# Optimization experiments

Measured on AMD Instinct MI355X. Metric: run time of the kernel, lower is better.

Reference implementation:

```python
import jax, jax.numpy as jnp
import numpy as np

D = 1024
H = 16
HD = D // H
FF = 4 * D
EPS = 1e-5


def setup_inputs() -> dict:
    key = jax.random.key(0)
    ks = jax.random.split(key, 16)
    s = lambda k, shape, scale: jax.random.normal(k, shape, dtype=jnp.float32) * scale
    inp = {
        "x": s(ks[0], (8, 1024, D), 1.0),
        "Wq": s(ks[1], (D, D), D ** -0.5), "bq": jnp.zeros((D,), jnp.float32),
        "Wk": s(ks[2], (D, D), D ** -0.5), "bk": jnp.zeros((D,), jnp.float32),
        "Wv": s(ks[3], (D, D), D ** -0.5), "bv": jnp.zeros((D,), jnp.float32),
        "Wo": s(ks[4], (D, D), D ** -0.5), "bo": jnp.zeros((D,), jnp.float32),
        "W1": s(ks[5], (D, FF), D ** -0.5), "b1": jnp.zeros((FF,), jnp.float32),
        "W2": s(ks[6], (FF, D), FF ** -0.5), "b2": jnp.zeros((D,), jnp.float32),
        "g1": jnp.ones((D,), jnp.float32), "be1": jnp.zeros((D,), jnp.float32),
        "g2": jnp.ones((D,), jnp.float32), "be2": jnp.zeros((D,), jnp.float32),
    }
    return inp


def _layernorm(x, g, b):
    mu = jnp.mean(x, axis=-1, keepdims=True)
    var = jnp.var(x, axis=-1, keepdims=True)
    return (x - mu) * jax.lax.rsqrt(var + EPS) * g + b


def reference(x, Wq, bq, Wk, bk, Wv, bv, Wo, bo, W1, b1, W2, b2, g1, be1, g2, be2):
    B, S, _ = x.shape
    # --- pre-norm attention block (dropout = identity in eval) ---
    h = _layernorm(x, g1, be1)
    q = (h @ Wq + bq).reshape(B, S, H, HD)
    k = (h @ Wk + bk).reshape(B, S, H, HD)
    v = (h @ Wv + bv).reshape(B, S, H, HD)
    scores = jnp.einsum('bqhd,bkhd->bhqk', q, k) / jnp.sqrt(jnp.float32(HD))
    attn = jax.nn.softmax(scores, axis=-1)
    ctx = jnp.einsum('bhqk,bkhd->bqhd', attn, v).reshape(B, S, D)
    x = x + (ctx @ Wo + bo)
    # --- pre-norm FFN block ---
    h = _layernorm(x, g2, be2)
    h = jax.nn.gelu(h @ W1 + b1, approximate=False)
    x = x + (h @ W2 + b2)
    return x
```

## Files before the change

### kernel.cpp

```cpp
#include <hip/hip_runtime.h>
#include <hip/hip_bf16.h>
#include <math.h>
#include <stdint.h>

typedef unsigned short u16;
typedef unsigned int u32;
typedef __attribute__((ext_vector_type(8))) short short8;
typedef __attribute__((ext_vector_type(4))) float f32x4;

__device__ __forceinline__ float b2f(u16 u) {
  union { u32 i; float f; } v; v.i = ((u32)u) << 16; return v.f;
}
__device__ __forceinline__ u16 f2b(float f) {
  union { float f; u32 i; } v; v.f = f;
  return (u16)((v.i + 0x7FFFu + ((v.i >> 16) & 1u)) >> 16);
}

__device__ __forceinline__ void gload_lds16(const u16* g, u16* l) {
  __builtin_amdgcn_global_load_lds((const __attribute__((address_space(1))) void*)g,
                                   (__attribute__((address_space(3))) void*)l, 16, 0, 0);
}

#define LD8(p) (*(const short8*)(p))
#define MFMA_BF16 __builtin_amdgcn_mfma_f32_16x16x32_bf16

__global__ __launch_bounds__(256) void transpose_k(const float* __restrict__ in,
                                                   u16* __restrict__ out, int K, int N) {
  __shared__ u16 tile[32][33];
  int n0 = blockIdx.x * 32, k0 = blockIdx.y * 32;
  int tx = threadIdx.x & 31, ty = threadIdx.x >> 5;
  #pragma unroll
  for (int i = ty; i < 32; i += 8)
    tile[i][tx] = f2b(in[(size_t)(k0 + i) * N + n0 + tx]);
  __syncthreads();
  #pragma unroll
  for (int i = ty; i < 32; i += 8)
    out[(size_t)(n0 + i) * K + k0 + tx] = tile[tx][i];
}

__global__ __launch_bounds__(256) void cat3_k(const float* __restrict__ a, const float* __restrict__ b,
                                              const float* __restrict__ c, float* __restrict__ o) {
  int i = blockIdx.x * 256 + threadIdx.x;
  o[i] = i < 1024 ? a[i] : (i < 2048 ? b[i - 1024] : c[i - 2048]);
}

__global__ __launch_bounds__(256) void vtrans_k(const u16* __restrict__ qkv, u16* __restrict__ vt) {
  __shared__ u16 tile[32][33];
  int bh = blockIdx.y, b = bh >> 4, h = bh & 15;
  int s0 = (blockIdx.x & 31) * 32, d0 = (blockIdx.x >> 5) * 32;
  int tx = threadIdx.x & 31, ty = threadIdx.x >> 5;
  #pragma unroll
  for (int i = ty; i < 32; i += 8)
    tile[i][tx] = qkv[(size_t)(b * 1024 + s0 + i) * 3072 + 2048 + h * 64 + d0 + tx];
  __syncthreads();
  #pragma unroll
  for (int i = ty; i < 32; i += 8)
    vt[(size_t)(bh * 64 + d0 + i) * 1024 + s0 + tx] = tile[tx][i];
}

template<int FP32IN>
__global__ __launch_bounds__(256) void ln_k(const void* __restrict__ xv, const float* __restrict__ g,
                                            const float* __restrict__ be, u16* __restrict__ out) {
  int row = blockIdx.x, t = threadIdx.x;
  float f0, f1, f2, f3;
  if (FP32IN) {
    const float* xr = (const float*)xv + (size_t)row * 1024;
    float4 x4 = *(const float4*)(xr + t * 4);
    f0 = x4.x; f1 = x4.y; f2 = x4.z; f3 = x4.w;
  } else {
    const u16* xr = (const u16*)xv + (size_t)row * 1024;
    ushort4 x4 = *(const ushort4*)(xr + t * 4);
    f0 = b2f(x4.x); f1 = b2f(x4.y); f2 = b2f(x4.z); f3 = b2f(x4.w);
  }
  float s = f0 + f1 + f2 + f3;
  float ss = f0 * f0 + f1 * f1 + f2 * f2 + f3 * f3;
  #pragma unroll
  for (int off = 32; off > 0; off >>= 1) { s += __shfl_down(s, off); ss += __shfl_down(ss, off); }
  __shared__ float sb[4], ssb[4];
  if ((t & 63) == 0) { sb[t >> 6] = s; ssb[t >> 6] = ss; }
  __syncthreads();
  s = sb[0] + sb[1] + sb[2] + sb[3];
  ss = ssb[0] + ssb[1] + ssb[2] + ssb[3];
  float mu = s * (1.0f / 1024.0f);
  float var = ss * (1.0f / 1024.0f) - mu * mu;
  float rstd = rsqrtf(var + 1e-5f);
  float4 gv = *(const float4*)(g + t * 4);
  float4 bv = *(const float4*)(be + t * 4);
  ushort4 o;
  o.x = f2b((f0 - mu) * rstd * gv.x + bv.x);
  o.y = f2b((f1 - mu) * rstd * gv.y + bv.y);
  o.z = f2b((f2 - mu) * rstd * gv.z + bv.z);
  o.w = f2b((f3 - mu) * rstd * gv.w + bv.w);
  *(ushort4*)(out + (size_t)row * 1024 + t * 4) = o;
}

template<int ACT, int RESID, int OUTF32>
__global__ __launch_bounds__(256) void gemm_k(const u16* __restrict__ A, const u16* __restrict__ Bt,
                                              const float* __restrict__ bias, const void* __restrict__ resid,
                                              void* __restrict__ Cv, int M, int N, int K, int ldc) {
  __shared__ u16 As[2][128 * 32];
  __shared__ u16 Bs[2][128 * 32];
  int Ny = N >> 7;
  int lin = blockIdx.y * 64 + blockIdx.x;
  int c8 = lin & 7, sblk = lin >> 3;
  int mq = sblk / Ny;
  int m0 = ((mq << 3) | c8) << 7;
  int n0 = (sblk - mq * Ny) << 7;
  int t = threadIdx.x;
  int wave = t >> 6, lane = t & 63, quad = lane >> 4, l16 = lane & 15;
  int wm = (wave >> 1) * 64, wn = (wave & 1) * 64;
  f32x4 acc[4][4] = {};
  int lr = lane >> 2;
  int lc = (lane & 3) ^ ((lane >> 3) & 3);
  const u16* Ab = A + (size_t)(m0 + wave * 16 + lr) * K + lc * 8;
  const u16* Bb = Bt + (size_t)(n0 + wave * 16 + lr) * K + lc * 8;
  const int lb = wave * 16 * 32;
  const int rdoff = (quad ^ ((l16 >> 1) & 3)) * 8;
  #pragma unroll
  for (int i = 0; i < 2; i++) {
    gload_lds16(Ab + (size_t)i * 64 * K, &As[0][lb + i * 64 * 32]);
    gload_lds16(Bb + (size_t)i * 64 * K, &Bs[0][lb + i * 64 * 32]);
  }
  const int niter = K >> 5;
  for (int c = 0; c < niter; c++) {
    int buf = c & 1;
    __syncthreads();
    if (c + 1 < niter) {
      int k1 = (c + 1) << 5;
      #pragma unroll
      for (int i = 0; i < 2; i++) {
        gload_lds16(Ab + k1 + (size_t)i * 64 * K, &As[buf ^ 1][lb + i * 64 * 32]);
        gload_lds16(Bb + k1 + (size_t)i * 64 * K, &Bs[buf ^ 1][lb + i * 64 * 32]);
      }
    }
    short8 a[4], b[4];
    #pragma unroll
    for (int i = 0; i < 4; i++)
      a[i] = LD8(&As[buf][(wm + i * 16 + l16) * 32 + rdoff]);
    #pragma unroll
    for (int j = 0; j < 4; j++)
      b[j] = LD8(&Bs[buf][(wn + j * 16 + l16) * 32 + rdoff]);
    #pragma unroll
    for (int i = 0; i < 4; i++)
      #pragma unroll
      for (int j = 0; j < 4; j++)
        acc[i][j] = MFMA_BF16(a[i], b[j], acc[i][j], 0, 0, 0);
  }
  float bcol[4];
  #pragma unroll
  for (int j = 0; j < 4; j++) bcol[j] = bias[n0 + wn + j * 16 + l16];
  #pragma unroll
  for (int i = 0; i < 4; i++) {
    #pragma unroll
    for (int r = 0; r < 4; r++) {
      int row = m0 + wm + i * 16 + quad * 4 + r;
      #pragma unroll
      for (int j = 0; j < 4; j++) {
        int col = n0 + wn + j * 16 + l16;
        float v = acc[i][j][r] + bcol[j];
        if (ACT == 1) {
          float e = v * (2.3022082f + 0.1029431f * v * v);
          float tt = exp2f(fminf(e, 80.0f));
          v = v * tt / (tt + 1.0f);
        }
        if (RESID == 1) v += b2f(((const u16*)resid)[(size_t)row * N + col]);
        if (RESID == 2) v += ((const float*)resid)[(size_t)row * N + col];
        if (OUTF32) ((float*)Cv)[(size_t)row * ldc + col] = v;
        else        ((u16*)Cv)[(size_t)row * ldc + col] = f2b(v);
      }
    }
  }
}

template<int ACT, int RESID, int OUTF32>
__global__ __launch_bounds__(512, 2) void gemm256_k(const u16* __restrict__ A, const u16* __restrict__ Bt,
                                                    const float* __restrict__ bias, const void* __restrict__ resid,
                                                    void* __restrict__ Cv, int M, int N, int K, int ldc) {
  __shared__ u16 As[2][256 * 64];
  __shared__ u16 Bs[2][256 * 64];
  int Ny = N >> 8;
  int lin = blockIdx.y * 32 + blockIdx.x;
  int c8 = lin & 7, sblk = lin >> 3;
  int mq = sblk / Ny;
  int m0 = ((mq << 3) | c8) << 8;
  int n0 = (sblk - mq * Ny) << 8;
  int t = threadIdx.x;
  int wave = t >> 6, lane = t & 63, quad = lane >> 4, l16 = lane & 15;
  int wm = (wave >> 2) << 7;
  int wn = (wave & 3) << 6;
  f32x4 acc[8][4] = {};
  int lrow = lane >> 3;
  int lchunk = (lane & 7) ^ lrow;
  const u16* Ab = A + (size_t)(m0 + wave * 32 + lrow) * K + lchunk * 8;
  const u16* Bb = Bt + (size_t)(n0 + wave * 32 + lrow) * K + lchunk * 8;
  const int sbase = wave * 32 * 64;
  const int x7 = l16 & 7;
  const int rdA = (wm + l16) * 64;
  const int rdB = (wn + l16) * 64;
  const int cz0 = (quad ^ x7) * 8;
  const int cz1 = ((4 + quad) ^ x7) * 8;
  const int niter = K >> 6;
  #pragma unroll
  for (int g = 0; g < 4; g++) {
    gload_lds16(Ab + (size_t)g * 8 * K, &As[0][sbase + g * 8 * 64]);
    gload_lds16(Bb + (size_t)g * 8 * K, &Bs[0][sbase + g * 8 * 64]);
  }
  asm volatile("s_waitcnt vmcnt(0)" ::: "memory");
  __builtin_amdgcn_s_barrier();
  __builtin_amdgcn_sched_barrier(0);
  for (int tt = 0; tt < niter; tt++) {
    int buf = tt & 1;
    const bool pf = (tt + 1 < niter);
    const int kpf = (tt + 1) << 6;
    const u16* Ac = &As[buf][0];
    const u16* Bc = &Bs[buf][0];
    u16* Aw = &As[buf ^ 1][0];
    u16* Bw = &Bs[buf ^ 1][0];
    short8 a0, a1, a2, a3, a4, a5, a6, a7, b0, b1, b2, b3;
    a0 = LD8(Ac + rdA + cz0);
    a1 = LD8(Ac + rdA + 1024 + cz0);
    a2 = LD8(Ac + rdA + 2048 + cz0);
    a3 = LD8(Ac + rdA + 3072 + cz0);
    b0 = LD8(Bc + rdB + cz0);
    b1 = LD8(Bc + rdB + 1024 + cz0);
    b2 = LD8(Bc + rdB + 2048 + cz0);
    b3 = LD8(Bc + rdB + 3072 + cz0);
    if (pf) {
      #pragma unroll
      for (int g = 0; g < 4; g++)
        gload_lds16(Ab + kpf + (size_t)g * 8 * K, Aw + sbase + g * 8 * 64);
    }
    __builtin_amdgcn_s_barrier();
    asm volatile("s_waitcnt lgkmcnt(0)" ::: "memory");
    __builtin_amdgcn_sched_barrier(0);
    __builtin_amdgcn_s_setprio(1);
    acc[0][0] = MFMA_BF16(a0, b0, acc[0][0], 0, 0, 0);
    acc[0][1] = MFMA_BF16(a0, b1, acc[0][1], 0, 0, 0);
    acc[0][2] = MFMA_BF16(a0, b2, acc[0][2], 0, 0, 0);
    acc[0][3] = MFMA_BF16(a0, b3, acc[0][3], 0, 0, 0);
    acc[1][0] = MFMA_BF16(a1, b0, acc[1][0], 0, 0, 0);
    acc[1][1] = MFMA_BF16(a1, b1, acc[1][1], 0, 0, 0);
    acc[1][2] = MFMA_BF16(a1, b2, acc[1][2], 0, 0, 0);
    acc[1][3] = MFMA_BF16(a1, b3, acc[1][3], 0, 0, 0);
    acc[2][0] = MFMA_BF16(a2, b0, acc[2][0], 0, 0, 0);
    acc[2][1] = MFMA_BF16(a2, b1, acc[2][1], 0, 0, 0);
    acc[2][2] = MFMA_BF16(a2, b2, acc[2][2], 0, 0, 0);
    acc[2][3] = MFMA_BF16(a2, b3, acc[2][3], 0, 0, 0);
    acc[3][0] = MFMA_BF16(a3, b0, acc[3][0], 0, 0, 0);
    acc[3][1] = MFMA_BF16(a3, b1, acc[3][1], 0, 0, 0);
    acc[3][2] = MFMA_BF16(a3, b2, acc[3][2], 0, 0, 0);
    acc[3][3] = MFMA_BF16(a3, b3, acc[3][3], 0, 0, 0);
    __builtin_amdgcn_s_setprio(0);
    __builtin_amdgcn_s_barrier();
    __builtin_amdgcn_sched_barrier(0);
    a4 = LD8(Ac + rdA + 4096 + cz0);
    a5 = LD8(Ac + rdA + 5120 + cz0);
    a6 = LD8(Ac + rdA + 6144 + cz0);
    a7 = LD8(Ac + rdA + 7168 + cz0);
    if (pf) {
      #pragma unroll
      for (int g = 0; g < 4; g++)
        gload_lds16(Bb + kpf + (size_t)g * 8 * K, Bw + sbase + g * 8 * 64);
    }
    __builtin_amdgcn_s_barrier();
    asm volatile("s_waitcnt lgkmcnt(0)" ::: "memory");
    __builtin_amdgcn_sched_barrier(0);
    __builtin_amdgcn_s_setprio(1);
    acc[4][0] = MFMA_BF16(a4, b0, acc[4][0], 0, 0, 0);
    acc[4][1] = MFMA_BF16(a4, b1, acc[4][1], 0, 0, 0);
    acc[4][2] = MFMA_BF16(a4, b2, acc[4][2], 0, 0, 0);
    acc[4][3] = MFMA_BF16(a4, b3, acc[4][3], 0, 0, 0);
    acc[5][0] = MFMA_BF16(a5, b0, acc[5][0], 0, 0, 0);
    acc[5][1] = MFMA_BF16(a5, b1, acc[5][1], 0, 0, 0);
    acc[5][2] = MFMA_BF16(a5, b2, acc[5][2], 0, 0, 0);
    acc[5][3] = MFMA_BF16(a5, b3, acc[5][3], 0, 0, 0);
    acc[6][0] = MFMA_BF16(a6, b0, acc[6][0], 0, 0, 0);
    acc[6][1] = MFMA_BF16(a6, b1, acc[6][1], 0, 0, 0);
    acc[6][2] = MFMA_BF16(a6, b2, acc[6][2], 0, 0, 0);
    acc[6][3] = MFMA_BF16(a6, b3, acc[6][3], 0, 0, 0);
    acc[7][0] = MFMA_BF16(a7, b0, acc[7][0], 0, 0, 0);
    acc[7][1] = MFMA_BF16(a7, b1, acc[7][1], 0, 0, 0);
    acc[7][2] = MFMA_BF16(a7, b2, acc[7][2], 0, 0, 0);
    acc[7][3] = MFMA_BF16(a7, b3, acc[7][3], 0, 0, 0);
    __builtin_amdgcn_s_setprio(0);
    __builtin_amdgcn_s_barrier();
    __builtin_amdgcn_sched_barrier(0);
    a0 = LD8(Ac + rdA + cz1);
    a1 = LD8(Ac + rdA + 1024 + cz1);
    a2 = LD8(Ac + rdA + 2048 + cz1);
    a3 = LD8(Ac + rdA + 3072 + cz1);
    b0 = LD8(Bc + rdB + cz1);
    b1 = LD8(Bc + rdB + 1024 + cz1);
    b2 = LD8(Bc + rdB + 2048 + cz1);
    b3 = LD8(Bc + rdB + 3072 + cz1);
    __builtin_amdgcn_s_barrier();
    asm volatile("s_waitcnt lgkmcnt(0)" ::: "memory");
    __builtin_amdgcn_sched_barrier(0);
    __builtin_amdgcn_s_setprio(1);
    acc[0][0] = MFMA_BF16(a0, b0, acc[0][0], 0, 0, 0);
    acc[0][1] = MFMA_BF16(a0, b1, acc[0][1], 0, 0, 0);
    acc[0][2] = MFMA_BF16(a0, b2, acc[0][2], 0, 0, 0);
    acc[0][3] = MFMA_BF16(a0, b3, acc[0][3], 0, 0, 0);
    acc[1][0] = MFMA_BF16(a1, b0, acc[1][0], 0, 0, 0);
    acc[1][1] = MFMA_BF16(a1, b1, acc[1][1], 0, 0, 0);
    acc[1][2] = MFMA_BF16(a1, b2, acc[1][2], 0, 0, 0);
    acc[1][3] = MFMA_BF16(a1, b3, acc[1][3], 0, 0, 0);
    acc[2][0] = MFMA_BF16(a2, b0, acc[2][0], 0, 0, 0);
    acc[2][1] = MFMA_BF16(a2, b1, acc[2][1], 0, 0, 0);
    acc[2][2] = MFMA_BF16(a2, b2, acc[2][2], 0, 0, 0);
    acc[2][3] = MFMA_BF16(a2, b3, acc[2][3], 0, 0, 0);
    acc[3][0] = MFMA_BF16(a3, b0, acc[3][0], 0, 0, 0);
    acc[3][1] = MFMA_BF16(a3, b1, acc[3][1], 0, 0, 0);
    acc[3][2] = MFMA_BF16(a3, b2, acc[3][2], 0, 0, 0);
    acc[3][3] = MFMA_BF16(a3, b3, acc[3][3], 0, 0, 0);
    __builtin_amdgcn_s_setprio(0);
    __builtin_amdgcn_s_barrier();
    __builtin_amdgcn_sched_barrier(0);
    a4 = LD8(Ac + rdA + 4096 + cz1);
    a5 = LD8(Ac + rdA + 5120 + cz1);
    a6 = LD8(Ac + rdA + 6144 + cz1);
    a7 = LD8(Ac + rdA + 7168 + cz1);
    __builtin_amdgcn_s_barrier();
    asm volatile("s_waitcnt lgkmcnt(0)" ::: "memory");
    __builtin_amdgcn_sched_barrier(0);
    __builtin_amdgcn_s_setprio(1);
    acc[4][0] = MFMA_BF16(a4, b0, acc[4][0], 0, 0, 0);
    acc[4][1] = MFMA_BF16(a4, b1, acc[4][1], 0, 0, 0);
    acc[4][2] = MFMA_BF16(a4, b2, acc[4][2], 0, 0, 0);
    acc[4][3] = MFMA_BF16(a4, b3, acc[4][3], 0, 0, 0);
    acc[5][0] = MFMA_BF16(a5, b0, acc[5][0], 0, 0, 0);
    acc[5][1] = MFMA_BF16(a5, b1, acc[5][1], 0, 0, 0);
    acc[5][2] = MFMA_BF16(a5, b2, acc[5][2], 0, 0, 0);
    acc[5][3] = MFMA_BF16(a5, b3, acc[5][3], 0, 0, 0);
    acc[6][0] = MFMA_BF16(a6, b0, acc[6][0], 0, 0, 0);
    acc[6][1] = MFMA_BF16(a6, b1, acc[6][1], 0, 0, 0);
    acc[6][2] = MFMA_BF16(a6, b2, acc[6][2], 0, 0, 0);
    acc[6][3] = MFMA_BF16(a6, b3, acc[6][3], 0, 0, 0);
    acc[7][0] = MFMA_BF16(a7, b0, acc[7][0], 0, 0, 0);
    acc[7][1] = MFMA_BF16(a7, b1, acc[7][1], 0, 0, 0);
    acc[7][2] = MFMA_BF16(a7, b2, acc[7][2], 0, 0, 0);
    acc[7][3] = MFMA_BF16(a7, b3, acc[7][3], 0, 0, 0);
    __builtin_amdgcn_s_setprio(0);
    if (pf) {
      asm volatile("s_waitcnt vmcnt(0)" ::: "memory");
      __builtin_amdgcn_s_barrier();
      __builtin_amdgcn_sched_barrier(0);
    }
  }
  float bcol[4];
  #pragma unroll
  for (int j = 0; j < 4; j++) bcol[j] = bias[n0 + wn + j * 16 + l16];
  #pragma unroll
  for (int i = 0; i < 8; i++) {
    #pragma unroll
    for (int r = 0; r < 4; r++) {
      int row = m0 + wm + i * 16 + quad * 4 + r;
      #pragma unroll
      for (int j = 0; j < 4; j++) {
        int col = n0 + wn + j * 16 + l16;
        float v = acc[i][j][r] + bcol[j];
        if (ACT == 1) {
          float e = v * (2.3022082f + 0.1029431f * v * v);
          float tt2 = exp2f(fminf(e, 80.0f));
          v = v * tt2 / (tt2 + 1.0f);
        }
        if (RESID == 1) v += b2f(((const u16*)resid)[(size_t)row * N + col]);
        if (RESID == 2) v += ((const float*)resid)[(size_t)row * N + col];
        if (OUTF32) ((float*)Cv)[(size_t)row * ldc + col] = v;
        else        ((u16*)Cv)[(size_t)row * ldc + col] = f2b(v);
      }
    }
  }
}

__global__ __launch_bounds__(256) void attn_k(const u16* __restrict__ QKV, const u16* __restrict__ VT,
                                              u16* __restrict__ ctx) {
  int bh = blockIdx.x;
  int b = bh >> 4;
  int q0 = blockIdx.y * 64;
  int t = threadIdx.x, wave = t >> 6, lane = t & 63, quad = lane >> 4, l16 = lane & 15;
  __shared__ u16 Ks[2][64 * 64];
  __shared__ u16 Vs[2][64 * 64];
  __shared__ u16 Plds[4][16][72];
  const size_t base = ((size_t)b * 1024) * 3072 + (size_t)(bh & 15) * 64;
  const u16* Kbase = QKV + base + 1024;
  const u16* vtb = VT + (size_t)bh * 64 * 1024;
  int lrow = lane >> 3;
  int lchunk = (lane & 7) ^ (lrow & 7);
  int srow = wave * 16;
  short8 qa[2];
  #pragma unroll
  for (int kh = 0; kh < 2; kh++)
    qa[kh] = *(const short8*)(QKV + base + (size_t)(q0 + wave * 16 + l16) * 3072 + kh * 32 + quad * 8);
  #pragma unroll
  for (int half = 0; half < 2; half++) {
    int r8 = srow + half * 8;
    gload_lds16(Kbase + (size_t)(r8 + lrow) * 3072 + lchunk * 8, &Ks[0][r8 * 64]);
    gload_lds16(vtb + (size_t)(r8 + lrow) * 1024 + lchunk * 8, &Vs[0][r8 * 64]);
  }
  f32x4 o[4] = {};
  float l_acc[4] = {0.f, 0.f, 0.f, 0.f};
  for (int c = 0; c < 16; c++) {
    int buf = c & 1;
    __syncthreads();
    if (c < 15) {
      #pragma unroll
      for (int half = 0; half < 2; half++) {
        int r8 = srow + half * 8;
        gload_lds16(Kbase + (size_t)((c + 1) * 64 + r8 + lrow) * 3072 + lchunk * 8, &Ks[buf ^ 1][r8 * 64]);
        gload_lds16(vtb + (size_t)(r8 + lrow) * 1024 + (c + 1) * 64 + lchunk * 8, &Vs[buf ^ 1][r8 * 64]);
      }
    }
    f32x4 s[4] = {};
    #pragma unroll
    for (int kh = 0; kh < 2; kh++)
      #pragma unroll
      for (int j = 0; j < 4; j++) {
        int row = j * 16 + l16;
        int pc = (kh * 4 + quad) ^ (row & 7);
        short8 kb = *(const short8*)(&Ks[buf][row * 64 + pc * 8]);
        s[j] = MFMA_BF16(qa[kh], kb, s[j], 0, 0, 0);
      }
    #pragma unroll
    for (int j = 0; j < 4; j++)
      #pragma unroll
      for (int r = 0; r < 4; r++) {
        float p = exp2f(s[j][r] * 0.18033688011112042f);
        l_acc[r] += p;
        Plds[wave][quad * 4 + r][j * 16 + l16] = f2b(p);
      }
    #pragma unroll
    for (int kh = 0; kh < 2; kh++) {
      short8 pa = *(const short8*)(&Plds[wave][l16][kh * 32 + quad * 8]);
      #pragma unroll
      for (int d4 = 0; d4 < 4; d4++) {
        int row = d4 * 16 + l16;
        int pc = (kh * 4 + quad) ^ (row & 7);
        short8 vb = *(const short8*)(&Vs[buf][row * 64 + pc * 8]);
        o[d4] = MFMA_BF16(pa, vb, o[d4], 0, 0, 0);
      }
    }
  }
  #pragma unroll
  for (int off = 1; off < 16; off <<= 1)
    #pragma unroll
    for (int r = 0; r < 4; r++) l_acc[r] += __shfl_xor(l_acc[r], off);
  #pragma unroll
  for (int r = 0; r < 4; r++) {
    float inv = 1.0f / l_acc[r];
    size_t row = (size_t)b * 1024 + q0 + wave * 16 + quad * 4 + r;
    #pragma unroll
    for (int d4 = 0; d4 < 4; d4++) {
      int col = (bh & 15) * 64 + d4 * 16 + l16;
      ctx[row * 1024 + col] = f2b(o[d4][r] * inv);
    }
  }
}

extern "C" void kernel_launch(void* const* d_in, const int* in_sizes, int n_in,
                              void* d_out, int out_size, void* d_ws, size_t ws_size,
                              hipStream_t stream) {
  const float* x   = (const float*)d_in[0];
  const float* Wq  = (const float*)d_in[1];  const float* bq  = (const float*)d_in[2];
  const float* Wk  = (const float*)d_in[3];  const float* bk  = (const float*)d_in[4];
  const float* Wv  = (const float*)d_in[5];  const float* bv  = (const float*)d_in[6];
  const float* Wo  = (const float*)d_in[7];  const float* bo  = (const float*)d_in[8];
  const float* W1  = (const float*)d_in[9];  const float* b1  = (const float*)d_in[10];
  const float* W2  = (const float*)d_in[11]; const float* b2  = (const float*)d_in[12];
  const float* g1  = (const float*)d_in[13]; const float* be1 = (const float*)d_in[14];
  const float* g2  = (const float*)d_in[15]; const float* be2 = (const float*)d_in[16];

  char* ws = (char*)d_ws;
  const size_t MB = 1024 * 1024;
  u16* h1    = (u16*)(ws + 0 * MB);
  u16* qkv   = (u16*)(ws + 16 * MB);
  u16* x1    = (u16*)(ws + 16 * MB);
  u16* h2    = (u16*)(ws + 32 * MB);
  u16* W2T   = (u16*)(ws + 48 * MB);
  u16* WqkvT = (u16*)(ws + 64 * MB);
  u16* WoT   = (u16*)(ws + 70 * MB);
  u16* W1T   = (u16*)(ws + 72 * MB);
  float* bqkv = (float*)(ws + 80 * MB);
  u16* h3f   = (u16*)(ws + 80 * MB);
  u16* vt    = h1;
  u16* ctx   = (u16*)d_out;
  float* out = (float*)d_out;

  transpose_k<<<dim3(32, 32), 256, 0, stream>>>(Wq, WqkvT, 1024, 1024);
  transpose_k<<<dim3(32, 32), 256, 0, stream>>>(Wk, WqkvT + (size_t)1024 * 1024, 1024, 1024);
  transpose_k<<<dim3(32, 32), 256, 0, stream>>>(Wv, WqkvT + (size_t)2048 * 1024, 1024, 1024);
  transpose_k<<<dim3(32, 32), 256, 0, stream>>>(Wo, WoT, 1024, 1024);
  transpose_k<<<dim3(128, 32), 256, 0, stream>>>(W1, W1T, 1024, 4096);
  cat3_k<<<12, 256, 0, stream>>>(bq, bk, bv, bqkv);

  ln_k<1><<<8192, 256, 0, stream>>>(x, g1, be1, h1);

  gemm256_k<0, 0, 0><<<dim3(32, 12), 512, 0, stream>>>(h1, WqkvT, bqkv, nullptr, qkv,
                                                       8192, 3072, 1024, 3072);

  vtrans_k<<<dim3(64, 128), 256, 0, stream>>>(qkv, vt);

  attn_k<<<dim3(128, 16), 256, 0, stream>>>(qkv, vt, ctx);

  gemm_k<0, 2, 0><<<dim3(64, 8), 256, 0, stream>>>(ctx, WoT, bo, x, x1,
                                                   8192, 1024, 1024, 1024);

  transpose_k<<<dim3(32, 128), 256, 0, stream>>>(W2, W2T, 4096, 1024);

  ln_k<0><<<8192, 256, 0, stream>>>(x1, g2, be2, h2);

  gemm256_k<1, 0, 0><<<dim3(32, 16), 512, 0, stream>>>(h2, W1T, b1, nullptr, h3f,
                                                       8192, 4096, 1024, 4096);
  gemm_k<0, 1, 1><<<dim3(64, 8), 256, 0, stream>>>(h3f, W2T, b2, x1, out,
                                                   8192, 1024, 4096, 1024);

  (void)in_sizes; (void)n_in; (void)out_size; (void)ws_size;
}
```

Before: 537.0 us.

## Replace 128x128 GEMM with 256x128 triple-buffered pipelined kernel for N=1024 GEMMs

Adds a new GEMM kernel with 256x128 tiles, 512 threads, K-step 64, three-stage LDS buffering via direct global-to-LDS loads, XOR-swizzled LDS layout, explicit barriers/waitcnt and setprio around MFMA clusters. It replaces the old 128x128 kernel for the output projection and FFN down projection. The intent is to overlap global loads with MFMA work and improve per-block data reuse. The cost is much larger LDS use (144KB), which limits occupancy, and 256 blocks for these GEMMs, which barely covers the CUs.

```diff
diff --git a/kernel.cpp b/kernel.cpp
--- a/kernel.cpp
+++ b/kernel.cpp
@@ -92,84 +92,6 @@
   o.z = f2b((f2 - mu) * rstd * gv.z + bv.z);
   o.w = f2b((f3 - mu) * rstd * gv.w + bv.w);
   *(ushort4*)(out + (size_t)row * 1024 + t * 4) = o;
-}
-
-template<int ACT, int RESID, int OUTF32>
-__global__ __launch_bounds__(256) void gemm_k(const u16* __restrict__ A, const u16* __restrict__ Bt,
-                                              const float* __restrict__ bias, const void* __restrict__ resid,
-                                              void* __restrict__ Cv, int M, int N, int K, int ldc) {
-  __shared__ u16 As[2][128 * 32];
-  __shared__ u16 Bs[2][128 * 32];
-  int Ny = N >> 7;
-  int lin = blockIdx.y * 64 + blockIdx.x;
-  int c8 = lin & 7, sblk = lin >> 3;
-  int mq = sblk / Ny;
-  int m0 = ((mq << 3) | c8) << 7;
-  int n0 = (sblk - mq * Ny) << 7;
-  int t = threadIdx.x;
-  int wave = t >> 6, lane = t & 63, quad = lane >> 4, l16 = lane & 15;
-  int wm = (wave >> 1) * 64, wn = (wave & 1) * 64;
-  f32x4 acc[4][4] = {};
-  int lr = lane >> 2;
-  int lc = (lane & 3) ^ ((lane >> 3) & 3);
-  const u16* Ab = A + (size_t)(m0 + wave * 16 + lr) * K + lc * 8;
-  const u16* Bb = Bt + (size_t)(n0 + wave * 16 + lr) * K + lc * 8;
-  const int lb = wave * 16 * 32;
-  const int rdoff = (quad ^ ((l16 >> 1) & 3)) * 8;
-  #pragma unroll
-  for (int i = 0; i < 2; i++) {
-    gload_lds16(Ab + (size_t)i * 64 * K, &As[0][lb + i * 64 * 32]);
-    gload_lds16(Bb + (size_t)i * 64 * K, &Bs[0][lb + i * 64 * 32]);
-  }
-  const int niter = K >> 5;
-  for (int c = 0; c < niter; c++) {
-    int buf = c & 1;
-    __syncthreads();
-    if (c + 1 < niter) {
-      int k1 = (c + 1) << 5;
-      #pragma unroll
-      for (int i = 0; i < 2; i++) {
-        gload_lds16(Ab + k1 + (size_t)i * 64 * K, &As[buf ^ 1][lb + i * 64 * 32]);
-        gload_lds16(Bb + k1 + (size_t)i * 64 * K, &Bs[buf ^ 1][lb + i * 64 * 32]);
-      }
-    }
-    short8 a[4], b[4];
-    #pragma unroll
-    for (int i = 0; i < 4; i++)
-      a[i] = LD8(&As[buf][(wm + i * 16 + l16) * 32 + rdoff]);
-    #pragma unroll
-    for (int j = 0; j < 4; j++)
-      b[j] = LD8(&Bs[buf][(wn + j * 16 + l16) * 32 + rdoff]);
-    #pragma unroll
-    for (int i = 0; i < 4; i++)
-      #pragma unroll
-      for (int j = 0; j < 4; j++)
-        acc[i][j] = MFMA_BF16(a[i], b[j], acc[i][j], 0, 0, 0);
-  }
-  float bcol[4];
-  #pragma unroll
-  for (int j = 0; j < 4; j++) bcol[j] = bias[n0 + wn + j * 16 + l16];
-  #pragma unroll
-  for (int i = 0; i < 4; i++) {
-    #pragma unroll
-    for (int r = 0; r < 4; r++) {
-      int row = m0 + wm + i * 16 + quad * 4 + r;
-      #pragma unroll
-      for (int j = 0; j < 4; j++) {
-        int col = n0 + wn + j * 16 + l16;
-        float v = acc[i][j][r] + bcol[j];
-        if (ACT == 1) {
-          float e = v * (2.3022082f + 0.1029431f * v * v);
-          float tt = exp2f(fminf(e, 80.0f));
-          v = v * tt / (tt + 1.0f);
-        }
-        if (RESID == 1) v += b2f(((const u16*)resid)[(size_t)row * N + col]);
-        if (RESID == 2) v += ((const float*)resid)[(size_t)row * N + col];
-        if (OUTF32) ((float*)Cv)[(size_t)row * ldc + col] = v;
-        else        ((u16*)Cv)[(size_t)row * ldc + col] = f2b(v);
-      }
-    }
-  }
 }
 
 template<int ACT, int RESID, int OUTF32>
@@ -373,6 +295,162 @@
   }
 }
 
+template<int ACT, int RESID, int OUTF32>
+__global__ __launch_bounds__(512, 2) void gemm256n_k(const u16* __restrict__ A, const u16* __restrict__ Bt,
+                                                     const float* __restrict__ bias, const void* __restrict__ resid,
+                                                     void* __restrict__ Cv, int M, int N, int K, int ldc) {
+  __shared__ u16 As[3][256 * 64];
+  __shared__ u16 Bs[3][128 * 64];
+  int Ny = N >> 7;
+  int lin = blockIdx.y * 32 + blockIdx.x;
+  int c8 = lin & 7, sblk = lin >> 3;
+  int mq = sblk / Ny;
+  int m0 = ((mq << 3) | c8) << 8;
+  int n0 = (sblk - mq * Ny) << 7;
+  int t = threadIdx.x;
+  int wave = t >> 6, lane = t & 63, quad = lane >> 4, l16 = lane & 15;
+  int wm = (wave >> 1) << 6;
+  int wn = (wave & 1) << 6;
+  f32x4 acc[4][4] = {};
+  int lrow = lane >> 3;
+  int lchunk = (lane & 7) ^ lrow;
+  const u16* Ab = A + (size_t)(m0 + wave * 32 + lrow) * K + lchunk * 8;
+  const u16* Bb = Bt + (size_t)(n0 + wave * 16 + lrow) * K + lchunk * 8;
+  const int sbA = wave * 32 * 64;
+  const int sbB = wave * 16 * 64;
+  const int x7 = l16 & 7;
+  const int rdA = (wm + l16) * 64;
+  const int rdB = (wn + l16) * 64;
+  const int cz0 = (quad ^ x7) * 8;
+  const int cz1 = ((4 + quad) ^ x7) * 8;
+  const int niter = K >> 6;
+  #pragma unroll
+  for (int p = 0; p < 2; p++) {
+    #pragma unroll
+    for (int g = 0; g < 4; g++)
+      gload_lds16(Ab + (p << 6) + (size_t)g * 8 * K, &As[p][sbA + g * 8 * 64]);
+    #pragma unroll
+    for (int g = 0; g < 2; g++)
+      gload_lds16(Bb + (p << 6) + (size_t)g * 8 * K, &Bs[p][sbB + g * 8 * 64]);
+  }
+  asm volatile("s_waitcnt vmcnt(6)" ::: "memory");
+  __builtin_amdgcn_s_barrier();
+  __builtin_amdgcn_sched_barrier(0);
+  int cur = 0;
+  for (int tt = 0; tt < niter; tt++) {
+    int wb = cur + 2; if (wb >= 3) wb -= 3;
+    const bool pf = (tt + 2 < niter);
+    const int kpf = (tt + 2) << 6;
+    const u16* Ac = &As[cur][0];
+    const u16* Bc = &Bs[cur][0];
+    short8 a0, a1, a2, a3, b0, b1, b2, b3;
+    a0 = LD8(Ac + rdA + cz0);
+    a1 = LD8(Ac + rdA + 1024 + cz0);
+    a2 = LD8(Ac + rdA + 2048 + cz0);
+    a3 = LD8(Ac + rdA + 3072 + cz0);
+    b0 = LD8(Bc + rdB + cz0);
+    b1 = LD8(Bc + rdB + 1024 + cz0);
+    b2 = LD8(Bc + rdB + 2048 + cz0);
+    b3 = LD8(Bc + rdB + 3072 + cz0);
+    if (pf) {
+      #pragma unroll
+      for (int g = 0; g < 4; g++)
+        gload_lds16(Ab + kpf + (size_t)g * 8 * K, &As[wb][sbA + g * 8 * 64]);
+    }
+    __builtin_amdgcn_s_barrier();
+    asm volatile("s_waitcnt lgkmcnt(0)" ::: "memory");
+    __builtin_amdgcn_sched_barrier(0);
+    __builtin_amdgcn_s_setprio(1);
+    acc[0][0] = MFMA_BF16(a0, b0, acc[0][0], 0, 0, 0);
+    acc[0][1] = MFMA_BF16(a0, b1, acc[0][1], 0, 0, 0);
+    acc[0][2] = MFMA_BF16(a0, b2, acc[0][2], 0, 0, 0);
+    acc[0][3] = MFMA_BF16(a0, b3, acc[0][3], 0, 0, 0);
+    acc[1][0] = MFMA_BF16(a1, b0, acc[1][0], 0, 0, 0);
+    acc[1][1] = MFMA_BF16(a1, b1, acc[1][1], 0, 0, 0);
+    acc[1][2] = MFMA_BF16(a1, b2, acc[1][2], 0, 0, 0);
+    acc[1][3] = MFMA_BF16(a1, b3, acc[1][3], 0, 0, 0);
+    acc[2][0] = MFMA_BF16(a2, b0, acc[2][0], 0, 0, 0);
+    acc[2][1] = MFMA_BF16(a2, b1, acc[2][1], 0, 0, 0);
+    acc[2][2] = MFMA_BF16(a2, b2, acc[2][2], 0, 0, 0);
+    acc[2][3] = MFMA_BF16(a2, b3, acc[2][3], 0, 0, 0);
+    acc[3][0] = MFMA_BF16(a3, b0, acc[3][0], 0, 0, 0);
+    acc[3][1] = MFMA_BF16(a3, b1, acc[3][1], 0, 0, 0);
+    acc[3][2] = MFMA_BF16(a3, b2, acc[3][2], 0, 0, 0);
+    acc[3][3] = MFMA_BF16(a3, b3, acc[3][3], 0, 0, 0);
+    __builtin_amdgcn_s_setprio(0);
+    __builtin_amdgcn_s_barrier();
+    __builtin_amdgcn_sched_barrier(0);
+    a0 = LD8(Ac + rdA + cz1);
+    a1 = LD8(Ac + rdA + 1024 + cz1);
+    a2 = LD8(Ac + rdA + 2048 + cz1);
+    a3 = LD8(Ac + rdA + 3072 + cz1);
+    b0 = LD8(Bc + rdB + cz1);
+    b1 = LD8(Bc + rdB + 1024 + cz1);
+    b2 = LD8(Bc + rdB + 2048 + cz1);
+    b3 = LD8(Bc + rdB + 3072 + cz1);
+    if (pf) {
+      #pragma unroll
+      for (int g = 0; g < 2; g++)
+        gload_lds16(Bb + kpf + (size_t)g * 8 * K, &Bs[wb][sbB + g * 8 * 64]);
+    }
+    __builtin_amdgcn_s_barrier();
+    asm volatile("s_waitcnt lgkmcnt(0)" ::: "memory");
+    __builtin_amdgcn_sched_barrier(0);
+    __builtin_amdgcn_s_setprio(1);
+    acc[0][0] = MFMA_BF16(a0, b0, acc[0][0], 0, 0, 0);
+    acc[0][1] = MFMA_BF16(a0, b1, acc[0][1], 0, 0, 0);
+    acc[0][2] = MFMA_BF16(a0, b2, acc[0][2], 0, 0, 0);
+    acc[0][3] = MFMA_BF16(a0, b3, acc[0][3], 0, 0, 0);
+    acc[1][0] = MFMA_BF16(a1, b0, acc[1][0], 0, 0, 0);
+    acc[1][1] = MFMA_BF16(a1, b1, acc[1][1], 0, 0, 0);
+    acc[1][2] = MFMA_BF16(a1, b2, acc[1][2], 0, 0, 0);
+    acc[1][3] = MFMA_BF16(a1, b3, acc[1][3], 0, 0, 0);
+    acc[2][0] = MFMA_BF16(a2, b0, acc[2][0], 0, 0, 0);
+    acc[2][1] = MFMA_BF16(a2, b1, acc[2][1], 0, 0, 0);
+    acc[2][2] = MFMA_BF16(a2, b2, acc[2][2], 0, 0, 0);
+    acc[2][3] = MFMA_BF16(a2, b3, acc[2][3], 0, 0, 0);
+    acc[3][0] = MFMA_BF16(a3, b0, acc[3][0], 0, 0, 0);
+    acc[3][1] = MFMA_BF16(a3, b1, acc[3][1], 0, 0, 0);
+    acc[3][2] = MFMA_BF16(a3, b2, acc[3][2], 0, 0, 0);
+    acc[3][3] = MFMA_BF16(a3, b3, acc[3][3], 0, 0, 0);
+    __builtin_amdgcn_s_setprio(0);
+    if (tt + 2 < niter) {
+      asm volatile("s_waitcnt vmcnt(6)" ::: "memory");
+    } else if (tt + 1 < niter) {
+      asm volatile("s_waitcnt vmcnt(0)" ::: "memory");
+    }
+    if (tt + 1 < niter) {
+      __builtin_amdgcn_s_barrier();
+      __builtin_amdgcn_sched_barrier(0);
+    }
+    cur = (cur == 2) ? 0 : cur + 1;
+  }
+  float bcol[4];
+  #pragma unroll
+  for (int j = 0; j < 4; j++) bcol[j] = bias[n0 + wn + j * 16 + l16];
+  #pragma unroll
+  for (int i = 0; i < 4; i++) {
+    #pragma unroll
+    for (int r = 0; r < 4; r++) {
+      int row = m0 + wm + i * 16 + quad * 4 + r;
+      #pragma unroll
+      for (int j = 0; j < 4; j++) {
+        int col = n0 + wn + j * 16 + l16;
+        float v = acc[i][j][r] + bcol[j];
+        if (ACT == 1) {
+          float e = v * (2.3022082f + 0.1029431f * v * v);
+          float tt2 = exp2f(fminf(e, 80.0f));
+          v = v * tt2 / (tt2 + 1.0f);
+        }
+        if (RESID == 1) v += b2f(((const u16*)resid)[(size_t)row * N + col]);
+        if (RESID == 2) v += ((const float*)resid)[(size_t)row * N + col];
+        if (OUTF32) ((float*)Cv)[(size_t)row * ldc + col] = v;
+        else        ((u16*)Cv)[(size_t)row * ldc + col] = f2b(v);
+      }
+    }
+  }
+}
+
 __global__ __launch_bounds__(256) void attn_k(const u16* __restrict__ QKV, const u16* __restrict__ VT,
                                               u16* __restrict__ ctx) {
   int bh = blockIdx.x;
@@ -502,8 +580,8 @@
 
   attn_k<<<dim3(128, 16), 256, 0, stream>>>(qkv, vt, ctx);
 
-  gemm_k<0, 2, 0><<<dim3(64, 8), 256, 0, stream>>>(ctx, WoT, bo, x, x1,
-                                                   8192, 1024, 1024, 1024);
+  gemm256n_k<0, 2, 0><<<dim3(32, 8), 512, 0, stream>>>(ctx, WoT, bo, x, x1,
+                                                       8192, 1024, 1024, 1024);
 
   transpose_k<<<dim3(32, 128), 256, 0, stream>>>(W2, W2T, 4096, 1024);
 
@@ -511,8 +589,8 @@
 
   gemm256_k<1, 0, 0><<<dim3(32, 16), 512, 0, stream>>>(h2, W1T, b1, nullptr, h3f,
                                                        8192, 4096, 1024, 4096);
-  gemm_k<0, 1, 1><<<dim3(64, 8), 256, 0, stream>>>(h3f, W2T, b2, x1, out,
-                                                   8192, 1024, 4096, 1024);
+  gemm256n_k<0, 1, 1><<<dim3(32, 8), 512, 0, stream>>>(h3f, W2T, b2, x1, out,
+                                                       8192, 1024, 4096, 1024);
 
   (void)in_sizes; (void)n_in; (void)out_size; (void)ws_size;
 }
```

Result: faster. 515.4 us (-4.0%).
